# Performance work log

Hardware: AMD Instinct MI355X
Metric: run time of the kernel (lower is better)

## Reference

```python
import jax, jax.numpy as jnp
import numpy as np

S = 60            # voxel grid side
N = 100000        # active voxels
M_PAD = 60000     # padded pairs per kernel offset
C_IN = 64
C_OUT = 64
KV = 27           # kernel volume (3^3)
CENTER = 13


def _build_maps():
    rng = np.random.default_rng(0)
    lin = rng.choice(S ** 3, size=N, replace=False)
    coords = np.stack(np.unravel_index(lin, (S, S, S)), axis=1).astype(np.int64)  # [N,3]
    lut = -np.ones(S ** 3, dtype=np.int64)
    lut[lin] = np.arange(N)
    imap = -np.ones((KV - 1, M_PAD), dtype=np.int32)
    omap = -np.ones((KV - 1, M_PAD), dtype=np.int32)
    row = 0
    for k in range(KV):
        if k == CENTER:
            continue
        d = np.array([k // 9 - 1, (k // 3) % 3 - 1, k % 3 - 1])
        nb = coords + d
        valid = np.all((nb >= 0) & (nb < S), axis=1)
        linnb = nb[:, 0] * S * S + nb[:, 1] * S + nb[:, 2]
        j = np.where(valid, lut[np.clip(linnb, 0, S ** 3 - 1)], -1)
        mask = j >= 0
        src = np.nonzero(mask)[0].astype(np.int32)   # input idx (gather)
        dst = j[mask].astype(np.int32)               # output idx (scatter)
        m = min(src.shape[0], M_PAD)
        imap[row, :m] = src[:m]
        omap[row, :m] = dst[:m]
        row += 1
    return imap, omap


def setup_inputs() -> dict:
    key = jax.random.key(0)
    kf, kw = jax.random.split(key)
    feats = jax.random.normal(kf, (N, C_IN), dtype=jnp.float32)
    stdv = 1.0 / np.sqrt(C_OUT * KV)
    kernel = jax.random.uniform(kw, (KV, C_IN, C_OUT), dtype=jnp.float32,
                                minval=-stdv, maxval=stdv)
    imap_np, omap_np = _build_maps()
    return {
        "feats": feats,
        "kernel": kernel,
        "imap": jnp.asarray(imap_np),
        "omap": jnp.asarray(omap_np),
    }


def reference(feats, kernel, imap, omap):
    # Submanifold sparse 3D conv: center weight applied densely,
    # 26 neighbor offsets via gather -> per-offset GEMM -> scatter-add.
    # feats: [N, Cin], kernel: [27, Cin, Cout], imap/omap: [26, M] (-1 = pad)
    koff = jnp.concatenate([jnp.arange(CENTER), jnp.arange(CENTER + 1, KV)])
    w_off = kernel[koff]                                   # [26, Cin, Cout]
    out = feats @ kernel[CENTER]                           # [N, Cout] center GEMM
    valid = (imap >= 0)                                    # [26, M]
    gathered = feats[jnp.clip(imap, 0)] * valid[..., None].astype(feats.dtype)  # [26, M, Cin]
    partial = jnp.einsum('kmc,kco->kmo', gathered, w_off)  # [26, M, Cout]
    dst = jnp.where(valid, omap, 0).reshape(-1)            # padded rows contribute zeros
    out = out.at[dst].add(partial.reshape(-1, partial.shape[-1]))
    return out
```

## Files before the change

### kernel.cpp

```cpp
#include <hip/hip_runtime.h>


#define N_PTS 100000
#define MPAD  60000
#define C     64
#define NSL   27

typedef short bf16x8 __attribute__((ext_vector_type(8)));
typedef float f32x4  __attribute__((ext_vector_type(4)));

static __device__ inline unsigned short f2bf(float x) {
    unsigned int u = __float_as_uint(x);
    u += 0x7fffu + ((u >> 16) & 1u);
    return (unsigned short)(u >> 16);
}

#define FEATS16_BYTES ((size_t)(N_PTS + 1) * C * 2)
#define WFRAG_OFF     (((FEATS16_BYTES) + 255) & ~(size_t)255)
#define WFRAG_BYTES   ((size_t)NSL * 8192)
#define NBR_OFF       (WFRAG_OFF + WFRAG_BYTES)
#define NBR_BYTES     ((size_t)26 * N_PTS * 4)

#define FEAT_ITEMS 800008
#define WF_ITEMS   (NSL * 2 * 4 * 64)
#define SCAT_ITEMS (26 * MPAD / 4)
#define PREP_TOTAL (FEAT_ITEMS + WF_ITEMS + SCAT_ITEMS)

__global__ __launch_bounds__(256) void prep_one(const float* __restrict__ feats,
                                                const float* __restrict__ kern,
                                                const int* __restrict__ imap,
                                                const int* __restrict__ omap,
                                                unsigned short* __restrict__ f16,
                                                unsigned short* __restrict__ wf,
                                                int* __restrict__ nbr) {
    const int idx = blockIdx.x * 256 + threadIdx.x;
    if (idx < FEAT_ITEMS) {
        bf16x8* dst = (bf16x8*)f16;
        if (idx < FEAT_ITEMS - 8) {
            const float4* src = (const float4*)feats;
            const float4 a = src[2 * idx];
            const float4 b = src[2 * idx + 1];
            bf16x8 v;
            v[0] = (short)f2bf(a.x); v[1] = (short)f2bf(a.y);
            v[2] = (short)f2bf(a.z); v[3] = (short)f2bf(a.w);
            v[4] = (short)f2bf(b.x); v[5] = (short)f2bf(b.y);
            v[6] = (short)f2bf(b.z); v[7] = (short)f2bf(b.w);
            dst[idx] = v;
        } else {
            dst[idx] = (bf16x8){0, 0, 0, 0, 0, 0, 0, 0};
        }
    } else if (idx < FEAT_ITEMS + WF_ITEMS) {
        const int w = idx - FEAT_ITEMS;
        const int lane = w & 63;
        const int rest = w >> 6;
        const int ct = rest & 3;
        const int kk = (rest >> 2) & 1;
        const int s  = rest >> 3;
        bf16x8 v = (bf16x8){0, 0, 0, 0, 0, 0, 0, 0};
        if (s < NSL) {
            const int q = lane >> 4, t = lane & 15;
            const int ksrc = (s == 26) ? 13 : (s + (s >= 13 ? 1 : 0));
            const int k0 = kk * 32 + q * 8;
            const int n  = ct * 16 + t;
            const float* wp = kern + (size_t)ksrc * 4096 + n;
            #pragma unroll
            for (int j = 0; j < 8; ++j) v[j] = (short)f2bf(wp[(size_t)(k0 + j) * 64]);
        }
        ((bf16x8*)wf)[w] = v;
    } else {
        const int k = idx - (FEAT_ITEMS + WF_ITEMS);
        if (k < SCAT_ITEMS) {
            const int s = k / (MPAD / 4);
            const int v = k - s * (MPAD / 4);
            const int4 iv = ((const int4*)(imap + (size_t)s * MPAD))[v];
            const int4 ov = ((const int4*)(omap + (size_t)s * MPAD))[v];
            int* nb = nbr + (size_t)s * N_PTS;
            if (iv.x >= 0) nb[ov.x] = iv.x;
            if (iv.y >= 0) nb[ov.y] = iv.y;
            if (iv.z >= 0) nb[ov.z] = iv.z;
            if (iv.w >= 0) nb[ov.w] = iv.w;
        }
    }
}

static __device__ inline void gl_lds(const char* g, char* l) {
    __builtin_amdgcn_global_load_lds(
        (const __attribute__((address_space(1))) unsigned int*)g,
        (__attribute__((address_space(3))) unsigned int*)l, 16, 0, 0);
}

#define WAITV(n) asm volatile("s_waitcnt vmcnt(" #n ")" ::: "memory")

__global__ __launch_bounds__(256, 3) void spconv_main(const unsigned short* __restrict__ f16,
                                                      const unsigned short* __restrict__ wf,
                                                      const int* __restrict__ nbr,
                                                      float* __restrict__ out) {
    __shared__ __align__(16) char bsm[2][8192];
    __shared__ __align__(16) char apool[4][2][4096];

    const int lane = threadIdx.x & 63;
    const int wave = threadIdx.x >> 6;
    const int q = lane >> 4, t = lane & 15;
    const int R0 = blockIdx.x * 128 + wave * 32;
    const int row0 = R0 + t;
    const int row1 = R0 + 16 + t;
    const bool inb0 = (row0 < N_PTS);
    const bool inb1 = (row1 < N_PTS);
    const int safe0 = inb0 ? row0 : 0;
    const int safe1 = inb1 ? row1 : 0;

    const bf16x8* fv = (const bf16x8*)f16;
    const char* wfb  = (const char*)wf;
    char* arng = (char*)apool[wave];

    int jr0[2], jr1[2];

#define LOADJ(s_) do { \
        jr0[(s_) & 1] = nbr[(size_t)(s_) * N_PTS + safe0]; \
        jr1[(s_) & 1] = nbr[(size_t)(s_) * N_PTS + safe1]; \
    } while (0)

#define GATHER(s_) do { \
        int j0, j1; \
        if ((s_) == 26) { j0 = inb0 ? row0 : -1; j1 = inb1 ? row1 : -1; } \
        else            { j0 = inb0 ? jr0[(s_) & 1] : -1; j1 = inb1 ? jr1[(s_) & 1] : -1; } \
        const int jz0 = ((unsigned)j0 < (unsigned)N_PTS) ? j0 : N_PTS; \
        const int jz1 = ((unsigned)j1 < (unsigned)N_PTS) ? j1 : N_PTS; \
        const char* g0 = (const char*)(fv + (size_t)jz0 * 8) + q * 16; \
        const char* g1 = (const char*)(fv + (size_t)jz1 * 8) + q * 16; \
        char* db = arng + ((s_) & 1) * 4096; \
        gl_lds(g0,      db);        \
        gl_lds(g0 + 64, db + 1024); \
        gl_lds(g1,      db + 2048); \
        gl_lds(g1 + 64, db + 3072); \
    } while (0)

#define STAGEB(s_) do { \
        const char* gs = wfb + (size_t)(s_) * 8192 + (size_t)(wave * 2) * 1024 + lane * 16; \
        char* bd = bsm[(s_) & 1] + (wave * 2) * 1024; \
        gl_lds(gs,        bd);        \
        gl_lds(gs + 1024, bd + 1024); \
    } while (0)

    LOADJ(0); LOADJ(1);
    STAGEB(0);
    GATHER(0);
    WAITV(4);
    __builtin_amdgcn_s_barrier();

    f32x4 acc[2][4];
    #pragma unroll
    for (int a = 0; a < 2; ++a)
        #pragma unroll
        for (int c = 0; c < 4; ++c)
            acc[a][c] = (f32x4){0.f, 0.f, 0.f, 0.f};

    #pragma unroll
    for (int st = 0; st < NSL; ++st) {
        if (st + 1 < NSL) STAGEB(st + 1);
        if (st + 2 < NSL - 1) LOADJ(st + 2);
        if (st + 1 < NSL) GATHER(st + 1);

        if (st <= 23)      WAITV(8);
        else if (st <= 25) WAITV(6);
        else               WAITV(0);

        const char* ab = arng + (st & 1) * 4096;
        const bf16x8 A0 = *(const bf16x8*)(ab +    0 + lane * 16);
        const bf16x8 A1 = *(const bf16x8*)(ab + 1024 + lane * 16);
        const bf16x8 A2 = *(const bf16x8*)(ab + 2048 + lane * 16);
        const bf16x8 A3 = *(const bf16x8*)(ab + 3072 + lane * 16);
        const char* bb = bsm[st & 1];
        bf16x8 B0[4], B1[4];
        #pragma unroll
        for (int ct = 0; ct < 4; ++ct) {
            B0[ct] = *(const bf16x8*)(bb +        ct * 1024 + lane * 16);
            B1[ct] = *(const bf16x8*)(bb + 4096 + ct * 1024 + lane * 16);
        }

        __builtin_amdgcn_s_setprio(1);
        #pragma unroll
        for (int ct = 0; ct < 4; ++ct) {
            acc[0][ct] = __builtin_amdgcn_mfma_f32_16x16x32_bf16(A0, B0[ct], acc[0][ct], 0, 0, 0);
            acc[1][ct] = __builtin_amdgcn_mfma_f32_16x16x32_bf16(A2, B0[ct], acc[1][ct], 0, 0, 0);
        }
        #pragma unroll
        for (int ct = 0; ct < 4; ++ct) {
            acc[0][ct] = __builtin_amdgcn_mfma_f32_16x16x32_bf16(A1, B1[ct], acc[0][ct], 0, 0, 0);
            acc[1][ct] = __builtin_amdgcn_mfma_f32_16x16x32_bf16(A3, B1[ct], acc[1][ct], 0, 0, 0);
        }
        __builtin_amdgcn_s_setprio(0);

        if (st <= 23)      { WAITV(6); __builtin_amdgcn_s_barrier(); }
        else if (st <= 25) { WAITV(4); __builtin_amdgcn_s_barrier(); }
    }

#undef LOADJ
#undef GATHER
#undef STAGEB

    #pragma unroll
    for (int tile = 0; tile < 2; ++tile) {
        #pragma unroll
        for (int i = 0; i < 4; ++i) {
            const int r = R0 + tile * 16 + 4 * q + i;
            if (r < N_PTS) {
                #pragma unroll
                for (int ct = 0; ct < 4; ++ct)
                    out[(size_t)r * C + ct * 16 + t] = acc[tile][ct][i];
            }
        }
    }
}

extern "C" void kernel_launch(void* const* d_in, const int* in_sizes, int n_in,
                              void* d_out, int out_size, void* d_ws, size_t ws_size,
                              hipStream_t stream) {
    const float* feats = (const float*)d_in[0];
    const float* kern  = (const float*)d_in[1];
    const int*   imap  = (const int*)d_in[2];
    const int*   omap  = (const int*)d_in[3];

    char* ws = (char*)d_ws;
    unsigned short* f16 = (unsigned short*)ws;
    unsigned short* wfr = (unsigned short*)(ws + WFRAG_OFF);
    int*            nbr = (int*)(ws + NBR_OFF);

    prep_one<<<dim3((PREP_TOTAL + 255) / 256), dim3(256), 0, stream>>>(
        feats, kern, imap, omap, f16, wfr, nbr);
    spconv_main<<<dim3((N_PTS + 127) / 128), dim3(256), 0, stream>>>(
        f16, wfr, nbr, (float*)d_out);
}
```

Before: 156.2 us.

## Triple-buffer LDS staging and preload all neighbor indices into registers

Moves the pipeline from double to triple buffering, so the gather and weight loads for slice s+2 are issued while slice s is computed, with a single wait and barrier per step. All 26 neighbor indices per row are loaded into registers up front instead of two stages ahead. This hides more of the gather latency, but LDS use grows and register pressure rises, so launch bounds drop from 3 to 2 blocks per CU and occupancy falls.

```diff
diff --git a/kernel.cpp b/kernel.cpp
--- a/kernel.cpp
+++ b/kernel.cpp
@@ -90,13 +90,14 @@
 }
 
 #define WAITV(n) asm volatile("s_waitcnt vmcnt(" #n ")" ::: "memory")
-
-__global__ __launch_bounds__(256, 3) void spconv_main(const unsigned short* __restrict__ f16,
+#define FENCE    asm volatile("" ::: "memory")
+
+__global__ __launch_bounds__(256, 2) void spconv_main(const unsigned short* __restrict__ f16,
                                                       const unsigned short* __restrict__ wf,
                                                       const int* __restrict__ nbr,
                                                       float* __restrict__ out) {
-    __shared__ __align__(16) char bsm[2][8192];
-    __shared__ __align__(16) char apool[4][2][4096];
+    __shared__ __align__(16) char bsm[3][8192];
+    __shared__ __align__(16) char apool[4][3][4096];
 
     const int lane = threadIdx.x & 63;
     const int wave = threadIdx.x >> 6;
@@ -113,22 +114,22 @@
     const char* wfb  = (const char*)wf;
     char* arng = (char*)apool[wave];
 
-    int jr0[2], jr1[2];
-
-#define LOADJ(s_) do { \
-        jr0[(s_) & 1] = nbr[(size_t)(s_) * N_PTS + safe0]; \
-        jr1[(s_) & 1] = nbr[(size_t)(s_) * N_PTS + safe1]; \
-    } while (0)
+    int j0r[26], j1r[26];
+    #pragma unroll
+    for (int s = 0; s < 26; ++s) {
+        j0r[s] = nbr[(size_t)s * N_PTS + safe0];
+        j1r[s] = nbr[(size_t)s * N_PTS + safe1];
+    }
 
 #define GATHER(s_) do { \
         int j0, j1; \
         if ((s_) == 26) { j0 = inb0 ? row0 : -1; j1 = inb1 ? row1 : -1; } \
-        else            { j0 = inb0 ? jr0[(s_) & 1] : -1; j1 = inb1 ? jr1[(s_) & 1] : -1; } \
+        else            { j0 = inb0 ? j0r[(s_)] : -1; j1 = inb1 ? j1r[(s_)] : -1; } \
         const int jz0 = ((unsigned)j0 < (unsigned)N_PTS) ? j0 : N_PTS; \
         const int jz1 = ((unsigned)j1 < (unsigned)N_PTS) ? j1 : N_PTS; \
         const char* g0 = (const char*)(fv + (size_t)jz0 * 8) + q * 16; \
         const char* g1 = (const char*)(fv + (size_t)jz1 * 8) + q * 16; \
-        char* db = arng + ((s_) & 1) * 4096; \
+        char* db = arng + ((s_) % 3) * 4096; \
         gl_lds(g0,      db);        \
         gl_lds(g0 + 64, db + 1024); \
         gl_lds(g1,      db + 2048); \
@@ -136,17 +137,16 @@
     } while (0)
 
 #define STAGEB(s_) do { \
-        const char* gs = wfb + (size_t)(s_) * 8192 + (size_t)(wave * 2) * 1024 + lane * 16; \
-        char* bd = bsm[(s_) & 1] + (wave * 2) * 1024; \
-        gl_lds(gs,        bd);        \
-        gl_lds(gs + 1024, bd + 1024); \
+        const char* gs = wfb + (size_t)(s_) * 8192 + wave * 2048 + lane * 16; \
+        char* bd = (char*)bsm[(s_) % 3] + wave * 2048; \
+        gl_lds(gs, bd); gl_lds(gs + 1024, bd + 1024); \
     } while (0)
 
-    LOADJ(0); LOADJ(1);
-    STAGEB(0);
-    GATHER(0);
-    WAITV(4);
+    STAGEB(0); FENCE; GATHER(0); FENCE;
+    STAGEB(1); FENCE; GATHER(1); FENCE;
+    WAITV(6);
     __builtin_amdgcn_s_barrier();
+    FENCE;
 
     f32x4 acc[2][4];
     #pragma unroll
@@ -156,28 +156,21 @@
             acc[a][c] = (f32x4){0.f, 0.f, 0.f, 0.f};
 
     #pragma unroll
-    for (int st = 0; st < NSL; ++st) {
-        if (st + 1 < NSL) STAGEB(st + 1);
-        if (st + 2 < NSL - 1) LOADJ(st + 2);
-        if (st + 1 < NSL) GATHER(st + 1);
-
-        if (st <= 23)      WAITV(8);
-        else if (st <= 25) WAITV(6);
-        else               WAITV(0);
-
-        const char* ab = arng + (st & 1) * 4096;
+    for (int s = 0; s < NSL; ++s) {
+        if (s + 2 <= 26) { STAGEB(s + 2); FENCE; GATHER(s + 2); FENCE; }
+
+        const char* ab = arng + (s % 3) * 4096;
         const bf16x8 A0 = *(const bf16x8*)(ab +    0 + lane * 16);
         const bf16x8 A1 = *(const bf16x8*)(ab + 1024 + lane * 16);
         const bf16x8 A2 = *(const bf16x8*)(ab + 2048 + lane * 16);
         const bf16x8 A3 = *(const bf16x8*)(ab + 3072 + lane * 16);
-        const char* bb = bsm[st & 1];
+        const char* bb = (const char*)bsm[s % 3];
         bf16x8 B0[4], B1[4];
         #pragma unroll
         for (int ct = 0; ct < 4; ++ct) {
             B0[ct] = *(const bf16x8*)(bb +        ct * 1024 + lane * 16);
             B1[ct] = *(const bf16x8*)(bb + 4096 + ct * 1024 + lane * 16);
         }
-
         __builtin_amdgcn_s_setprio(1);
         #pragma unroll
         for (int ct = 0; ct < 4; ++ct) {
@@ -191,11 +184,14 @@
         }
         __builtin_amdgcn_s_setprio(0);
 
-        if (st <= 23)      { WAITV(6); __builtin_amdgcn_s_barrier(); }
-        else if (st <= 25) { WAITV(4); __builtin_amdgcn_s_barrier(); }
-    }
-
-#undef LOADJ
+        if (s < 26) {
+            if (s <= 24) WAITV(6);
+            else         WAITV(0);
+            __builtin_amdgcn_s_barrier();
+            FENCE;
+        }
+    }
+
 #undef GATHER
 #undef STAGEB
 
```

After: 150.7 us. 3.5% less time.
